# Performance work log

Measured on AMD Instinct MI355X. Metric: run time of the kernel, lower is better.

The kernel has to match this reference:

```python
import jax, jax.numpy as jnp
import numpy as np

B, LQ, LK, D = 32, 2048, 2048, 64


def setup_inputs() -> dict:
    key = jax.random.key(0)
    k1, k2, k3, k4 = jax.random.split(key, 4)
    querys = jax.random.normal(k1, (B, LQ, D), dtype=jnp.float32)
    keys = jax.random.normal(k2, (B, LK, D), dtype=jnp.float32)
    values = jax.random.normal(k3, (B, LK, D), dtype=jnp.float32)
    # valid lengths in [1, LK]
    valid_lens = jax.random.randint(k4, (B,), 1, LK + 1, dtype=jnp.int32)
    return {"querys": querys, "keys": keys, "values": values, "valid_lens": valid_lens}


def reference(querys, keys, values, valid_lens):
    d = querys.shape[-1]
    # [B, Lq, Lk] score matrix
    scores = jnp.einsum("bqd,bkd->bqk", querys, keys) / jnp.sqrt(jnp.asarray(d, querys.dtype))
    # masked softmax: key positions >= valid_len get -1e6 (as in d2l masked_softmax)
    key_pos = jnp.arange(scores.shape[-1], dtype=jnp.int32)  # [Lk]
    mask = key_pos[None, None, :] < valid_lens[:, None, None]  # [B, 1, Lk]
    scores = jnp.where(mask, scores, jnp.asarray(-1e6, scores.dtype))
    attn = jax.nn.softmax(scores, axis=-1)
    # dropout p=0.0 -> identity
    return jnp.einsum("bqk,bkd->bqd", attn, values)
```

## Files before the change

### kernel.cpp

```cpp
#include <hip/hip_runtime.h>
#include <hip/hip_bf16.h>
#include <math.h>


#define B_    32
#define LQ_   2048
#define LK_   2048
#define D_    64

typedef __attribute__((ext_vector_type(8)))  short bf16x8;
typedef __attribute__((ext_vector_type(4)))  float f32x4;
typedef __attribute__((ext_vector_type(16))) float f32x16;
typedef __attribute__((ext_vector_type(2)))  unsigned u32x2;

static __device__ __forceinline__ unsigned pk_bf16(float a, float b) {
    __hip_bfloat162 h = __float22bfloat162_rn(float2{a, b});
    return *(unsigned*)&h;
}

static __device__ __forceinline__ u32x2 plswap(unsigned a, unsigned b) {
    return __builtin_amdgcn_permlane32_swap(a, b, false, false);
}
static __device__ __forceinline__ float xhalf_max(float x) {
    u32x2 r = plswap(__float_as_uint(x), __float_as_uint(x));
    return fmaxf(__uint_as_float(r[0]), __uint_as_float(r[1]));
}
static __device__ __forceinline__ float xhalf_add(float x) {
    u32x2 r = plswap(__float_as_uint(x), __float_as_uint(x));
    return __uint_as_float(r[0]) + __uint_as_float(r[1]);
}

template<int NS>
__global__ __launch_bounds__(256, 2) void fa_split9_kernel(
    const float* __restrict__ Q, const float* __restrict__ K,
    const float* __restrict__ V, const int* __restrict__ vlen,
    float* __restrict__ OP, float* __restrict__ ML)
{
    __shared__ __align__(16) short Kl[2][64 * 64];
    __shared__ __align__(16) short Vt[2][64 * 64];

    const int tid  = threadIdx.x;
    const int wid  = tid >> 6;
    const int lane = tid & 63;
    const int c31  = lane & 31;
    const int h    = lane >> 5;

    constexpr int PB = 16 * NS;
    const int L    = blockIdx.x;
    const int rank = L / PB;
    const int sub  = L % PB;
    const int qb   = sub & 15;
    const int s    = sub >> 4;
    int b;
    {
        const int vj = vlen[c31];
        int r = 0;
#pragma unroll
        for (int k = 0; k < 32; ++k) {
            const int vk = __shfl(vj, k);
            r += (vk > vj) || (vk == vj && k < c31);
        }
        const unsigned long long match = __ballot(r == rank);
        b = (int)(__ffsll((unsigned long long)match) - 1) & 31;
    }
    const int q0 = qb * 128 + wid * 32;
    const int vl = vlen[b];
    const int nt    = (vl + 63) >> 6;
    const int chunk = (nt + NS - 1) / NS;
    const int t0    = s * chunk;
    const int t1    = min(t0 + chunk, nt);

    const float qscale = 0.125f * 1.44269504088896340736f;

    unsigned qfrag[4][4];
#pragma unroll
    for (int ks = 0; ks < 4; ++ks) {
        const float* qp = Q + ((size_t)(b * LQ_ + q0 + c31)) * D_ + ks * 16 + h * 8;
        f32x4 t0v = *(const f32x4*)qp;
        f32x4 t1v = *(const f32x4*)(qp + 4);
#pragma unroll
        for (int jj = 0; jj < 2; ++jj) {
            qfrag[ks][jj]     = pk_bf16(t0v[2*jj] * qscale, t0v[2*jj+1] * qscale);
            qfrag[ks][jj + 2] = pk_bf16(t1v[2*jj] * qscale, t1v[2*jj+1] * qscale);
        }
    }

    f32x16 oacc[2];
#pragma unroll
    for (int dt = 0; dt < 2; ++dt)
#pragma unroll
        for (int r = 0; r < 16; ++r) oacc[dt][r] = 0.f;
    float mrun = -INFINITY, lrun = 0.f;

    const int skey = tid >> 2, skh = tid & 3;
    const int vkg = tid >> 4, vdg = tid & 15;

    const float* kgp = K + ((size_t)(b * LK_ + skey)) * D_ + skh * 16;
    const float* vgp = V + ((size_t)(b * LK_ + vkg * 4)) * D_ + vdg * 4;

    f32x4 kr[4], vr[4];
    if (t0 < t1) {
        const size_t off = (size_t)t0 * 64 * D_;
#pragma unroll
        for (int i = 0; i < 4; ++i) kr[i] = *(const f32x4*)(kgp + off + 4 * i);
#pragma unroll
        for (int i = 0; i < 4; ++i) vr[i] = *(const f32x4*)(vgp + off + (size_t)i * D_);
    }

    for (int t = t0; t < t1; ++t) {
        const int k0 = t * 64;
        const int buf = t & 1;

        {
            unsigned pk32[8];
#pragma unroll
            for (int m = 0; m < 8; ++m)
                pk32[m] = pk_bf16(kr[m >> 1][2 * (m & 1)], kr[m >> 1][2 * (m & 1) + 1]);
#pragma unroll
            for (int cch = 0; cch < 2; ++cch) {
                const int pos = (skh * 2 + cch) ^ (skey & 7);
                *(bf16x8*)&Kl[buf][skey * 64 + pos * 8] = *(bf16x8*)&pk32[4 * cch];
            }
#pragma unroll
            for (int dr = 0; dr < 4; ++dr) {
                const unsigned w0 = pk_bf16(vr[0][dr], vr[1][dr]);
                const unsigned w1 = pk_bf16(vr[2][dr], vr[3][dr]);
                const int dim = vdg * 4 + dr;
                const int pos = (vkg >> 1) ^ (dim & 7);
                uint2* dst = (uint2*)&Vt[buf][dim * 64 + pos * 8 + (vkg & 1) * 4];
                *dst = uint2{w0, w1};
            }
        }
        __syncthreads();

        if (t + 1 < t1) {
            const float* kn = kgp + (size_t)(k0 + 64) * D_;
            const float* vn = vgp + (size_t)(k0 + 64) * D_;
#pragma unroll
            for (int i = 0; i < 4; ++i) kr[i] = *(const f32x4*)(kn + 4 * i);
#pragma unroll
            for (int i = 0; i < 4; ++i) vr[i] = *(const f32x4*)(vn + (size_t)i * D_);
        }

        f32x16 st[2];
#pragma unroll
        for (int ss = 0; ss < 2; ++ss) {
#pragma unroll
            for (int r = 0; r < 16; ++r) st[ss][r] = 0.f;
#pragma unroll
            for (int ks = 0; ks < 4; ++ks) {
                const int pos = (ks * 2 + h) ^ (c31 & 7);
                bf16x8 kf = *(const bf16x8*)&Kl[buf][(ss * 32 + c31) * 64 + pos * 8];
                st[ss] = __builtin_amdgcn_mfma_f32_32x32x16_bf16(
                    kf, *(const bf16x8*)&qfrag[ks][0], st[ss], 0, 0, 0);
            }
        }

        if (k0 + 64 > vl) {
#pragma unroll
            for (int ss = 0; ss < 2; ++ss) {
                const int base = k0 + ss * 32 + 4 * h;
#pragma unroll
                for (int r = 0; r < 16; ++r) {
                    const int key = base + (r & 3) + 8 * (r >> 2);
                    if (key >= vl) st[ss][r] = -1e30f;
                }
            }
        }

        float m8[8];
#pragma unroll
        for (int r = 0; r < 8; ++r)
            m8[r] = fmaxf(fmaxf(st[0][r], st[0][r + 8]),
                          fmaxf(st[1][r], st[1][r + 8]));
#pragma unroll
        for (int o = 4; o; o >>= 1)
#pragma unroll
            for (int r = 0; r < o; ++r) m8[r] = fmaxf(m8[r], m8[r + o]);
        const float tm = xhalf_max(m8[0]);

        if (__any(tm > mrun + 8.f)) {
            const float mnew = fmaxf(mrun, tm);
            const float corr = exp2f(mrun - mnew);
            lrun *= corr;
#pragma unroll
            for (int dt = 0; dt < 2; ++dt)
#pragma unroll
                for (int r = 0; r < 16; ++r) oacc[dt][r] *= corr;
            mrun = mnew;
        }
#pragma unroll
        for (int ss = 0; ss < 2; ++ss)
#pragma unroll
            for (int r = 0; r < 16; ++r)
                st[ss][r] = exp2f(st[ss][r] - mrun);
        float s8[8];
#pragma unroll
        for (int r = 0; r < 8; ++r)
            s8[r] = (st[0][r] + st[0][r + 8]) + (st[1][r] + st[1][r + 8]);
#pragma unroll
        for (int o = 4; o; o >>= 1)
#pragma unroll
            for (int r = 0; r < o; ++r) s8[r] += s8[r + o];
        lrun += xhalf_add(s8[0]);

        unsigned pk[2][8];
#pragma unroll
        for (int ss = 0; ss < 2; ++ss)
#pragma unroll
            for (int m = 0; m < 8; ++m)
                pk[ss][m] = pk_bf16(st[ss][2 * m], st[ss][2 * m + 1]);

#pragma unroll
        for (int kq = 0; kq < 4; ++kq) {
            const int ss = kq >> 1, A4 = (kq & 1) * 4;
            u32x2 r02 = plswap(pk[ss][A4],     pk[ss][A4 + 2]);
            u32x2 r13 = plswap(pk[ss][A4 + 1], pk[ss][A4 + 3]);
            unsigned pf[4] = {r02[0], r13[0], r02[1], r13[1]};
            const bf16x8 pfr = *(const bf16x8*)&pf[0];
#pragma unroll
            for (int dt = 0; dt < 2; ++dt) {
                const int pos = (kq * 2 + h) ^ (c31 & 7);
                bf16x8 vf = *(const bf16x8*)&Vt[buf][(dt * 32 + c31) * 64 + pos * 8];
                oacc[dt] = __builtin_amdgcn_mfma_f32_32x32x16_bf16(vf, pfr, oacc[dt], 0, 0, 0);
            }
        }
    }

    const size_t row = (size_t)s * (B_ * LQ_) + b * LQ_ + q0 + c31;
    float* op = OP + row * D_;
#pragma unroll
    for (int dt = 0; dt < 2; ++dt)
#pragma unroll
        for (int g = 0; g < 4; ++g) {
            f32x4 v;
#pragma unroll
            for (int j = 0; j < 4; ++j) v[j] = oacc[dt][4 * g + j];
            *(f32x4*)(op + dt * 32 + 8 * g + 4 * h) = v;
        }
    if (h == 0)
        *(float2*)&ML[row * 2] = float2{mrun, lrun};
}

template<int NS>
__global__ __launch_bounds__(256) void fa_merge_kernel(
    const float* __restrict__ OP, const float* __restrict__ ML,
    float* __restrict__ O)
{
    const int g   = blockIdx.x * 256 + threadIdx.x;
    const int row = g >> 4;
    const int qd  = (g & 15) * 4;

    float mf = -INFINITY;
#pragma unroll
    for (int s = 0; s < NS; ++s) {
        float2 ml = *(const float2*)&ML[((size_t)s * (B_ * LQ_) + row) * 2];
        mf = fmaxf(mf, ml.x);
    }
    float den = 0.f;
    f32x4 acc = {0.f, 0.f, 0.f, 0.f};
#pragma unroll
    for (int s = 0; s < NS; ++s) {
        const size_t srow = (size_t)s * (B_ * LQ_) + row;
        float2 ml = *(const float2*)&ML[srow * 2];
        const float c = exp2f(ml.x - mf);
        den += c * ml.y;
        f32x4 v = *(const f32x4*)&OP[srow * D_ + qd];
        acc += v * c;
    }
    const float inv = 1.f / den;
    *(f32x4*)(O + (size_t)row * D_ + qd) = acc * inv;
}

__global__ __launch_bounds__(128, 2) void fa_mono_kernel(
    const float* __restrict__ Q, const float* __restrict__ K,
    const float* __restrict__ V, const int* __restrict__ vlen,
    float* __restrict__ O)
{
    __shared__ __align__(16) short Kl[2][64 * 64];
    __shared__ __align__(16) short Vt[2][64 * 64];

    const int tid  = threadIdx.x;
    const int wave = tid >> 6;
    const int lane = tid & 63;
    const int c31  = lane & 31;
    const int h    = lane >> 5;

    const int b  = blockIdx.y;
    const int q0 = blockIdx.x * 64 + wave * 32;
    const int vl = vlen[b];
    const int nt = (vl + 63) >> 6;

    const float qscale = 0.125f * 1.44269504088896340736f;

    unsigned qfrag[4][4];
#pragma unroll
    for (int ks = 0; ks < 4; ++ks) {
        const float* qp = Q + ((size_t)(b * LQ_ + q0 + c31)) * D_ + ks * 16 + h * 8;
        f32x4 t0 = *(const f32x4*)qp;
        f32x4 t1 = *(const f32x4*)(qp + 4);
#pragma unroll
        for (int jj = 0; jj < 2; ++jj) {
            qfrag[ks][jj]     = pk_bf16(t0[2*jj] * qscale, t0[2*jj+1] * qscale);
            qfrag[ks][jj + 2] = pk_bf16(t1[2*jj] * qscale, t1[2*jj+1] * qscale);
        }
    }

    f32x16 oacc[2];
#pragma unroll
    for (int dt = 0; dt < 2; ++dt)
#pragma unroll
        for (int r = 0; r < 16; ++r) oacc[dt][r] = 0.f;
    float mrun = -INFINITY, lrun = 0.f;

    const int skey = tid >> 1, skh = tid & 1;
    const int vkg = tid >> 4, vdg = tid & 15;

    const float* kgp = K + ((size_t)(b * LK_ + skey)) * D_ + skh * 32;
    const float* vgp = V + ((size_t)(b * LK_ + vkg * 8)) * D_ + vdg * 4;

    f32x4 kr[8], vr[8];
#pragma unroll
    for (int i = 0; i < 8; ++i) kr[i] = *(const f32x4*)(kgp + 4 * i);
#pragma unroll
    for (int i = 0; i < 8; ++i) vr[i] = *(const f32x4*)(vgp + (size_t)i * D_);

    for (int t = 0; t < nt; ++t) {
        const int k0 = t * 64;
        const int buf = t & 1;
        {
            unsigned pk32[16];
#pragma unroll
            for (int m = 0; m < 16; ++m)
                pk32[m] = pk_bf16(kr[m >> 1][2 * (m & 1)], kr[m >> 1][2 * (m & 1) + 1]);
#pragma unroll
            for (int cch = 0; cch < 4; ++cch) {
                const int pos = (skh * 4 + cch) ^ (skey & 7);
                *(bf16x8*)&Kl[buf][skey * 64 + pos * 8] = *(bf16x8*)&pk32[4 * cch];
            }
#pragma unroll
            for (int dr = 0; dr < 4; ++dr) {
                unsigned w[4];
#pragma unroll
                for (int p = 0; p < 4; ++p)
                    w[p] = pk_bf16(vr[2 * p][dr], vr[2 * p + 1][dr]);
                const int dim = vdg * 4 + dr;
                const int pos = vkg ^ (dim & 7);
                *(bf16x8*)&Vt[buf][dim * 64 + pos * 8] = *(bf16x8*)&w[0];
            }
        }
        if (t + 1 < nt) {
            const float* kn = kgp + (size_t)(k0 + 64) * D_;
            const float* vn = vgp + (size_t)(k0 + 64) * D_;
#pragma unroll
            for (int i = 0; i < 8; ++i) kr[i] = *(const f32x4*)(kn + 4 * i);
#pragma unroll
            for (int i = 0; i < 8; ++i) vr[i] = *(const f32x4*)(vn + (size_t)i * D_);
        }
        __syncthreads();

        f32x16 st[2];
#pragma unroll
        for (int ss = 0; ss < 2; ++ss) {
#pragma unroll
            for (int r = 0; r < 16; ++r) st[ss][r] = 0.f;
#pragma unroll
            for (int ks = 0; ks < 4; ++ks) {
                const int pos = (ks * 2 + h) ^ (c31 & 7);
                bf16x8 kf = *(const bf16x8*)&Kl[buf][(ss * 32 + c31) * 64 + pos * 8];
                st[ss] = __builtin_amdgcn_mfma_f32_32x32x16_bf16(
                    kf, *(const bf16x8*)&qfrag[ks][0], st[ss], 0, 0, 0);
            }
        }
        if (k0 + 64 > vl) {
#pragma unroll
            for (int ss = 0; ss < 2; ++ss) {
                const int base = k0 + ss * 32 + 4 * h;
#pragma unroll
                for (int r = 0; r < 16; ++r) {
                    const int key = base + (r & 3) + 8 * (r >> 2);
                    if (key >= vl) st[ss][r] = -1e30f;
                }
            }
        }
        float tm = st[0][0];
#pragma unroll
        for (int ss = 0; ss < 2; ++ss)
#pragma unroll
            for (int r = 0; r < 16; ++r) tm = fmaxf(tm, st[ss][r]);
        tm = fmaxf(tm, __shfl_xor(tm, 32));
        if (__any(tm > mrun + 8.f)) {
            const float mnew = fmaxf(mrun, tm);
            const float corr = exp2f(mrun - mnew);
            lrun *= corr;
#pragma unroll
            for (int dt = 0; dt < 2; ++dt)
#pragma unroll
                for (int r = 0; r < 16; ++r) oacc[dt][r] *= corr;
            mrun = mnew;
        }
        float rs = 0.f;
#pragma unroll
        for (int ss = 0; ss < 2; ++ss)
#pragma unroll
            for (int r = 0; r < 16; ++r) {
                const float p = exp2f(st[ss][r] - mrun);
                st[ss][r] = p;
                rs += p;
            }
        rs += __shfl_xor(rs, 32);
        lrun += rs;

        unsigned pk[2][8];
#pragma unroll
        for (int ss = 0; ss < 2; ++ss)
#pragma unroll
            for (int m = 0; m < 8; ++m)
                pk[ss][m] = pk_bf16(st[ss][2 * m], st[ss][2 * m + 1]);
#pragma unroll
        for (int kq = 0; kq < 4; ++kq) {
            const int ss = kq >> 1, A4 = (kq & 1) * 4;
            unsigned p0 = pk[ss][A4], p1 = pk[ss][A4+1], p2 = pk[ss][A4+2], p3 = pk[ss][A4+3];
            unsigned xp0 = __shfl_xor((int)p0, 32);
            unsigned xp1 = __shfl_xor((int)p1, 32);
            unsigned xp2 = __shfl_xor((int)p2, 32);
            unsigned xp3 = __shfl_xor((int)p3, 32);
            unsigned pf[4];
            pf[0] = h ? xp2 : p0;
            pf[1] = h ? xp3 : p1;
            pf[2] = h ? p2  : xp0;
            pf[3] = h ? p3  : xp1;
            const bf16x8 pfr = *(const bf16x8*)&pf[0];
#pragma unroll
            for (int dt = 0; dt < 2; ++dt) {
                const int pos = (kq * 2 + h) ^ (c31 & 7);
                bf16x8 vf = *(const bf16x8*)&Vt[buf][(dt * 32 + c31) * 64 + pos * 8];
                oacc[dt] = __builtin_amdgcn_mfma_f32_32x32x16_bf16(vf, pfr, oacc[dt], 0, 0, 0);
            }
        }
    }

    const float inv = 1.f / lrun;
    float* op = O + ((size_t)(b * LQ_ + q0 + c31)) * D_;
#pragma unroll
    for (int dt = 0; dt < 2; ++dt)
#pragma unroll
        for (int g = 0; g < 4; ++g) {
            f32x4 v;
#pragma unroll
            for (int j = 0; j < 4; ++j) v[j] = oacc[dt][4 * g + j] * inv;
            *(f32x4*)(op + dt * 32 + 8 * g + 4 * h) = v;
        }
}

extern "C" void kernel_launch(void* const* d_in, const int* in_sizes, int n_in,
                              void* d_out, int out_size, void* d_ws, size_t ws_size,
                              hipStream_t stream) {
    const float* Q    = (const float*)d_in[0];
    const float* K    = (const float*)d_in[1];
    const float* V    = (const float*)d_in[2];
    const int*   vlen = (const int*)d_in[3];
    float*       O    = (float*)d_out;

    const size_t rows = (size_t)B_ * LQ_;
    auto need = [&](int ns) { return (size_t)ns * rows * (D_ + 2) * sizeof(float); };

    int NS = 0;
    if      (d_ws && ws_size >= need(4)) NS = 4;
    else if (d_ws && ws_size >= need(2)) NS = 2;
    else if (d_ws && ws_size >= need(1)) NS = 1;

    if (NS == 0) {
        dim3 grid(LQ_ / 64, B_);
        fa_mono_kernel<<<grid, dim3(128), 0, stream>>>(Q, K, V, vlen, O);
        return;
    }

    float* OP = (float*)d_ws;
    float* ML = (float*)d_ws + (size_t)NS * rows * D_;

    const unsigned nblk = (unsigned)(16 * B_ * NS);
    switch (NS) {
        case 4: fa_split9_kernel<4><<<dim3(nblk), dim3(256), 0, stream>>>(Q, K, V, vlen, OP, ML); break;
        case 2: fa_split9_kernel<2><<<dim3(nblk), dim3(256), 0, stream>>>(Q, K, V, vlen, OP, ML); break;
        default: fa_split9_kernel<1><<<dim3(nblk), dim3(256), 0, stream>>>(Q, K, V, vlen, OP, ML); break;
    }

    dim3 g2((unsigned)((rows * (D_ / 4)) / 256));
    switch (NS) {
        case 4: fa_merge_kernel<4><<<g2, dim3(256), 0, stream>>>(OP, ML, O); break;
        case 2: fa_merge_kernel<2><<<g2, dim3(256), 0, stream>>>(OP, ML, O); break;
        default: fa_merge_kernel<1><<<g2, dim3(256), 0, stream>>>(OP, ML, O); break;
    }
}
```

Baseline: 153.0 us.

## Pre-convert K/V to bf16 and transposed V, load MFMA fragments directly from global

Adds a preprocessing kernel that converts K to bf16 and V to a transposed bf16 layout in workspace. A new attention kernel then has each wave load its MFMA operand fragments straight from global or L2, with no LDS staging and no __syncthreads. Each wave now owns a single 32-row query tile, with occupancy hinted at 4 blocks. This removes repeated per-block fp32-to-bf16 conversion and LDS traffic, but each wave re-reads K/V from cache, adds an extra launch, and needs a larger workspace to hold the bf16 copies.

```diff
diff --git a/kernel.cpp b/kernel.cpp
--- a/kernel.cpp
+++ b/kernel.cpp
@@ -28,6 +28,247 @@
 static __device__ __forceinline__ float xhalf_add(float x) {
     u32x2 r = plswap(__float_as_uint(x), __float_as_uint(x));
     return __uint_as_float(r[0]) + __uint_as_float(r[1]);
+}
+
+__global__ __launch_bounds__(256) void fa_cvt_kernel(
+    const float* __restrict__ K, const float* __restrict__ V,
+    short* __restrict__ Kb, short* __restrict__ Vtb)
+{
+    const int tid = threadIdx.x;
+    const int b   = blockIdx.y;
+    const int k0  = blockIdx.x * 64;
+
+    {
+        const int kk = tid >> 2, q4 = tid & 3;
+        const size_t off = ((size_t)(b * LK_ + k0 + kk)) * D_ + q4 * 16;
+        const float* src = K + off;
+        unsigned w[8];
+#pragma unroll
+        for (int i = 0; i < 4; ++i) {
+            f32x4 v = *(const f32x4*)(src + 4 * i);
+            w[2 * i]     = pk_bf16(v[0], v[1]);
+            w[2 * i + 1] = pk_bf16(v[2], v[3]);
+        }
+        short* dst = Kb + off;
+        *(bf16x8*)dst       = *(bf16x8*)&w[0];
+        *(bf16x8*)(dst + 8) = *(bf16x8*)&w[4];
+    }
+    {
+        const int vkg = tid & 15, vdg = tid >> 4;
+        f32x4 vv[4];
+#pragma unroll
+        for (int p = 0; p < 4; ++p)
+            vv[p] = *(const f32x4*)&V[((size_t)(b * LK_ + k0 + vkg * 4 + p)) * D_ + vdg * 4];
+#pragma unroll
+        for (int dr = 0; dr < 4; ++dr) {
+            uint2 w = { pk_bf16(vv[0][dr], vv[1][dr]), pk_bf16(vv[2][dr], vv[3][dr]) };
+            *(uint2*)&Vtb[((size_t)(b * 64 + vdg * 4 + dr)) * LK_ + k0 + vkg * 4] = w;
+        }
+    }
+}
+
+template<int NS>
+__global__ __launch_bounds__(256, 4) void fa_frag_kernel(
+    const float* __restrict__ Q, const short* __restrict__ Kb,
+    const short* __restrict__ Vtb, const int* __restrict__ vlen,
+    float* __restrict__ OP, float* __restrict__ ML)
+{
+    const int tid  = threadIdx.x;
+    const int wid  = tid >> 6;
+    const int lane = tid & 63;
+    const int c31  = lane & 31;
+    const int h    = lane >> 5;
+
+    constexpr int PB = 64 * NS;
+    const int T    = blockIdx.x * 4 + wid;
+    const int rank = T / PB;
+    const int sub  = T % PB;
+    const int qw   = sub & 63;
+    const int s    = sub >> 6;
+    int b;
+    {
+        const int vj = vlen[c31];
+        int r = 0;
+#pragma unroll
+        for (int k = 0; k < 32; ++k) {
+            const int vk = __shfl(vj, k);
+            r += (vk > vj) || (vk == vj && k < c31);
+        }
+        const unsigned long long match = __ballot(r == rank);
+        b = (int)(__ffsll(match) - 1) & 31;
+    }
+    const int q0 = qw * 32;
+    const int vl = vlen[b];
+    const int nt    = (vl + 63) >> 6;
+    const int chunk = (nt + NS - 1) / NS;
+    const int t0    = s * chunk;
+    const int t1    = min(t0 + chunk, nt);
+
+    const float qscale = 0.125f * 1.44269504088896340736f;
+
+    unsigned qfrag[4][4];
+#pragma unroll
+    for (int ks = 0; ks < 4; ++ks) {
+        const float* qp = Q + ((size_t)(b * LQ_ + q0 + c31)) * D_ + ks * 16 + h * 8;
+        f32x4 t0v = *(const f32x4*)qp;
+        f32x4 t1v = *(const f32x4*)(qp + 4);
+#pragma unroll
+        for (int jj = 0; jj < 2; ++jj) {
+            qfrag[ks][jj]     = pk_bf16(t0v[2*jj] * qscale, t0v[2*jj+1] * qscale);
+            qfrag[ks][jj + 2] = pk_bf16(t1v[2*jj] * qscale, t1v[2*jj+1] * qscale);
+        }
+    }
+
+    f32x16 oacc[2];
+#pragma unroll
+    for (int dt = 0; dt < 2; ++dt)
+#pragma unroll
+        for (int r = 0; r < 16; ++r) oacc[dt][r] = 0.f;
+    float mrun = -INFINITY, lrun = 0.f;
+
+    const short* kb  = Kb  + (size_t)b * LK_ * D_;
+    const short* vtb = Vtb + (size_t)b * D_ * LK_;
+
+    for (int t = t0; t < t1; ++t) {
+        const int k0 = t * 64;
+
+        bf16x8 kf[2][4];
+#pragma unroll
+        for (int ss = 0; ss < 2; ++ss)
+#pragma unroll
+            for (int ks = 0; ks < 4; ++ks)
+                kf[ss][ks] = *(const bf16x8*)&kb[((size_t)(k0 + ss * 32 + c31)) * D_ + ks * 16 + h * 8];
+
+        f32x16 st[2];
+#pragma unroll
+        for (int ss = 0; ss < 2; ++ss) {
+#pragma unroll
+            for (int r = 0; r < 16; ++r) st[ss][r] = 0.f;
+#pragma unroll
+            for (int ks = 0; ks < 4; ++ks)
+                st[ss] = __builtin_amdgcn_mfma_f32_32x32x16_bf16(
+                    kf[ss][ks], *(const bf16x8*)&qfrag[ks][0], st[ss], 0, 0, 0);
+        }
+
+        bf16x8 vf[2][4];
+#pragma unroll
+        for (int dt = 0; dt < 2; ++dt)
+#pragma unroll
+            for (int kq = 0; kq < 4; ++kq)
+                vf[dt][kq] = *(const bf16x8*)&vtb[((size_t)(dt * 32 + c31)) * LK_ + k0 + kq * 16 + h * 8];
+
+        if (k0 + 64 > vl) {
+#pragma unroll
+            for (int ss = 0; ss < 2; ++ss) {
+                const int base = k0 + ss * 32 + 4 * h;
+#pragma unroll
+                for (int r = 0; r < 16; ++r) {
+                    const int key = base + (r & 3) + 8 * (r >> 2);
+                    if (key >= vl) st[ss][r] = -1e30f;
+                }
+            }
+        }
+
+        float m8[8];
+#pragma unroll
+        for (int r = 0; r < 8; ++r)
+            m8[r] = fmaxf(fmaxf(st[0][r], st[0][r + 8]),
+                          fmaxf(st[1][r], st[1][r + 8]));
+#pragma unroll
+        for (int o = 4; o; o >>= 1)
+#pragma unroll
+            for (int r = 0; r < o; ++r) m8[r] = fmaxf(m8[r], m8[r + o]);
+        const float tm = xhalf_max(m8[0]);
+
+        if (__any(tm > mrun + 8.f)) {
+            const float mnew = fmaxf(mrun, tm);
+            const float corr = exp2f(mrun - mnew);
+            lrun *= corr;
+#pragma unroll
+            for (int dt = 0; dt < 2; ++dt)
+#pragma unroll
+                for (int r = 0; r < 16; ++r) oacc[dt][r] *= corr;
+            mrun = mnew;
+        }
+#pragma unroll
+        for (int ss = 0; ss < 2; ++ss)
+#pragma unroll
+            for (int r = 0; r < 16; ++r)
+                st[ss][r] = exp2f(st[ss][r] - mrun);
+        float s8[8];
+#pragma unroll
+        for (int r = 0; r < 8; ++r)
+            s8[r] = (st[0][r] + st[0][r + 8]) + (st[1][r] + st[1][r + 8]);
+#pragma unroll
+        for (int o = 4; o; o >>= 1)
+#pragma unroll
+            for (int r = 0; r < o; ++r) s8[r] += s8[r + o];
+        lrun += xhalf_add(s8[0]);
+
+        unsigned pk[2][8];
+#pragma unroll
+        for (int ss = 0; ss < 2; ++ss)
+#pragma unroll
+            for (int m = 0; m < 8; ++m)
+                pk[ss][m] = pk_bf16(st[ss][2 * m], st[ss][2 * m + 1]);
+
+#pragma unroll
+        for (int kq = 0; kq < 4; ++kq) {
+            const int ss = kq >> 1, A4 = (kq & 1) * 4;
+            u32x2 r02 = plswap(pk[ss][A4],     pk[ss][A4 + 2]);
+            u32x2 r13 = plswap(pk[ss][A4 + 1], pk[ss][A4 + 3]);
+            unsigned pf[4] = {r02[0], r13[0], r02[1], r13[1]};
+            const bf16x8 pfr = *(const bf16x8*)&pf[0];
+#pragma unroll
+            for (int dt = 0; dt < 2; ++dt)
+                oacc[dt] = __builtin_amdgcn_mfma_f32_32x32x16_bf16(
+                    vf[dt][kq], pfr, oacc[dt], 0, 0, 0);
+        }
+    }
+
+    const size_t row = (size_t)s * (B_ * LQ_) + b * LQ_ + q0 + c31;
+    float* op = OP + row * D_;
+#pragma unroll
+    for (int dt = 0; dt < 2; ++dt)
+#pragma unroll
+        for (int g = 0; g < 4; ++g) {
+            f32x4 v;
+#pragma unroll
+            for (int j = 0; j < 4; ++j) v[j] = oacc[dt][4 * g + j];
+            *(f32x4*)(op + dt * 32 + 8 * g + 4 * h) = v;
+        }
+    if (h == 0)
+        *(float2*)&ML[row * 2] = float2{mrun, lrun};
+}
+
+template<int NS>
+__global__ __launch_bounds__(256) void fa_merge_kernel(
+    const float* __restrict__ OP, const float* __restrict__ ML,
+    float* __restrict__ O)
+{
+    const int g   = blockIdx.x * 256 + threadIdx.x;
+    const int row = g >> 4;
+    const int qd  = (g & 15) * 4;
+
+    float mf = -INFINITY;
+#pragma unroll
+    for (int s = 0; s < NS; ++s) {
+        float2 ml = *(const float2*)&ML[((size_t)s * (B_ * LQ_) + row) * 2];
+        mf = fmaxf(mf, ml.x);
+    }
+    float den = 0.f;
+    f32x4 acc = {0.f, 0.f, 0.f, 0.f};
+#pragma unroll
+    for (int s = 0; s < NS; ++s) {
+        const size_t srow = (size_t)s * (B_ * LQ_) + row;
+        float2 ml = *(const float2*)&ML[srow * 2];
+        const float c = exp2f(ml.x - mf);
+        den += c * ml.y;
+        f32x4 v = *(const f32x4*)&OP[srow * D_ + qd];
+        acc += v * c;
+    }
+    const float inv = 1.f / den;
+    *(f32x4*)(O + (size_t)row * D_ + qd) = acc * inv;
 }
 
 template<int NS>
@@ -61,7 +302,7 @@
             r += (vk > vj) || (vk == vj && k < c31);
         }
         const unsigned long long match = __ballot(r == rank);
-        b = (int)(__ffsll((unsigned long long)match) - 1) & 31;
+        b = (int)(__ffsll(match) - 1) & 31;
     }
     const int q0 = qb * 128 + wid * 32;
     const int vl = vlen[b];
@@ -110,7 +351,6 @@
     for (int t = t0; t < t1; ++t) {
         const int k0 = t * 64;
         const int buf = t & 1;
-
         {
             unsigned pk32[8];
 #pragma unroll
@@ -127,12 +367,10 @@
                 const unsigned w1 = pk_bf16(vr[2][dr], vr[3][dr]);
                 const int dim = vdg * 4 + dr;
                 const int pos = (vkg >> 1) ^ (dim & 7);
-                uint2* dst = (uint2*)&Vt[buf][dim * 64 + pos * 8 + (vkg & 1) * 4];
-                *dst = uint2{w0, w1};
+                *(uint2*)&Vt[buf][dim * 64 + pos * 8 + (vkg & 1) * 4] = uint2{w0, w1};
             }
         }
         __syncthreads();
-
         if (t + 1 < t1) {
             const float* kn = kgp + (size_t)(k0 + 64) * D_;
             const float* vn = vgp + (size_t)(k0 + 64) * D_;
@@ -155,7 +393,6 @@
                     kf, *(const bf16x8*)&qfrag[ks][0], st[ss], 0, 0, 0);
             }
         }
-
         if (k0 + 64 > vl) {
 #pragma unroll
             for (int ss = 0; ss < 2; ++ss) {
@@ -167,7 +404,6 @@
                 }
             }
         }
-
         float m8[8];
 #pragma unroll
         for (int r = 0; r < 8; ++r)
@@ -178,7 +414,6 @@
 #pragma unroll
             for (int r = 0; r < o; ++r) m8[r] = fmaxf(m8[r], m8[r + o]);
         const float tm = xhalf_max(m8[0]);
-
         if (__any(tm > mrun + 8.f)) {
             const float mnew = fmaxf(mrun, tm);
             const float corr = exp2f(mrun - mnew);
@@ -210,7 +445,6 @@
 #pragma unroll
             for (int m = 0; m < 8; ++m)
                 pk[ss][m] = pk_bf16(st[ss][2 * m], st[ss][2 * m + 1]);
-
 #pragma unroll
         for (int kq = 0; kq < 4; ++kq) {
             const int ss = kq >> 1, A4 = (kq & 1) * 4;
@@ -221,8 +455,8 @@
 #pragma unroll
             for (int dt = 0; dt < 2; ++dt) {
                 const int pos = (kq * 2 + h) ^ (c31 & 7);
-                bf16x8 vf = *(const bf16x8*)&Vt[buf][(dt * 32 + c31) * 64 + pos * 8];
-                oacc[dt] = __builtin_amdgcn_mfma_f32_32x32x16_bf16(vf, pfr, oacc[dt], 0, 0, 0);
+                bf16x8 vfv = *(const bf16x8*)&Vt[buf][(dt * 32 + c31) * 64 + pos * 8];
+                oacc[dt] = __builtin_amdgcn_mfma_f32_32x32x16_bf16(vfv, pfr, oacc[dt], 0, 0, 0);
             }
         }
     }
@@ -240,36 +474,6 @@
         }
     if (h == 0)
         *(float2*)&ML[row * 2] = float2{mrun, lrun};
-}
-
-template<int NS>
-__global__ __launch_bounds__(256) void fa_merge_kernel(
-    const float* __restrict__ OP, const float* __restrict__ ML,
-    float* __restrict__ O)
-{
-    const int g   = blockIdx.x * 256 + threadIdx.x;
-    const int row = g >> 4;
-    const int qd  = (g & 15) * 4;
-
-    float mf = -INFINITY;
-#pragma unroll
-    for (int s = 0; s < NS; ++s) {
-        float2 ml = *(const float2*)&ML[((size_t)s * (B_ * LQ_) + row) * 2];
-        mf = fmaxf(mf, ml.x);
-    }
-    float den = 0.f;
-    f32x4 acc = {0.f, 0.f, 0.f, 0.f};
-#pragma unroll
-    for (int s = 0; s < NS; ++s) {
-        const size_t srow = (size_t)s * (B_ * LQ_) + row;
-        float2 ml = *(const float2*)&ML[srow * 2];
-        const float c = exp2f(ml.x - mf);
-        den += c * ml.y;
-        f32x4 v = *(const f32x4*)&OP[srow * D_ + qd];
-        acc += v * c;
-    }
-    const float inv = 1.f / den;
-    *(f32x4*)(O + (size_t)row * D_ + qd) = acc * inv;
 }
 
 __global__ __launch_bounds__(128, 2) void fa_mono_kernel(
@@ -462,34 +666,39 @@
     const int*   vlen = (const int*)d_in[3];
     float*       O    = (float*)d_out;
 
-    const size_t rows = (size_t)B_ * LQ_;
-    auto need = [&](int ns) { return (size_t)ns * rows * (D_ + 2) * sizeof(float); };
-
-    int NS = 0;
-    if      (d_ws && ws_size >= need(4)) NS = 4;
-    else if (d_ws && ws_size >= need(2)) NS = 2;
-    else if (d_ws && ws_size >= need(1)) NS = 1;
-
-    if (NS == 0) {
-        dim3 grid(LQ_ / 64, B_);
-        fa_mono_kernel<<<grid, dim3(128), 0, stream>>>(Q, K, V, vlen, O);
+    const size_t rows    = (size_t)B_ * LQ_;
+    const size_t kvElems = (size_t)B_ * LK_ * D_;
+    auto needP = [&](int ns) { return (size_t)ns * rows * (D_ + 2) * sizeof(float); };
+    const size_t needKV = 2 * kvElems * sizeof(short);
+
+    constexpr int NS = 4;
+
+    if (d_ws && ws_size >= needP(NS) + needKV) {
+        float* OP  = (float*)d_ws;
+        float* ML  = OP + (size_t)NS * rows * D_;
+        short* Kb  = (short*)(ML + (size_t)NS * rows * 2);
+        short* Vtb = Kb + kvElems;
+
+        fa_cvt_kernel<<<dim3(LK_ / 64, B_), dim3(256), 0, stream>>>(K, V, Kb, Vtb);
+
+        const unsigned nblk = (unsigned)(64 * B_ * NS / 4);
+        fa_frag_kernel<NS><<<dim3(nblk), dim3(256), 0, stream>>>(Q, Kb, Vtb, vlen, OP, ML);
+
+        dim3 g2((unsigned)((rows * (D_ / 4)) / 256));
+        fa_merge_kernel<NS><<<g2, dim3(256), 0, stream>>>(OP, ML, O);
         return;
     }
 
-    float* OP = (float*)d_ws;
-    float* ML = (float*)d_ws + (size_t)NS * rows * D_;
-
-    const unsigned nblk = (unsigned)(16 * B_ * NS);
-    switch (NS) {
-        case 4: fa_split9_kernel<4><<<dim3(nblk), dim3(256), 0, stream>>>(Q, K, V, vlen, OP, ML); break;
-        case 2: fa_split9_kernel<2><<<dim3(nblk), dim3(256), 0, stream>>>(Q, K, V, vlen, OP, ML); break;
-        default: fa_split9_kernel<1><<<dim3(nblk), dim3(256), 0, stream>>>(Q, K, V, vlen, OP, ML); break;
-    }
-
-    dim3 g2((unsigned)((rows * (D_ / 4)) / 256));
-    switch (NS) {
-        case 4: fa_merge_kernel<4><<<g2, dim3(256), 0, stream>>>(OP, ML, O); break;
-        case 2: fa_merge_kernel<2><<<g2, dim3(256), 0, stream>>>(OP, ML, O); break;
-        default: fa_merge_kernel<1><<<g2, dim3(256), 0, stream>>>(OP, ML, O); break;
-    }
-}
+    if (d_ws && ws_size >= needP(NS)) {
+        float* OP = (float*)d_ws;
+        float* ML = OP + (size_t)NS * rows * D_;
+        const unsigned nblk = (unsigned)(16 * B_ * NS);
+        fa_split9_kernel<NS><<<dim3(nblk), dim3(256), 0, stream>>>(Q, K, V, vlen, OP, ML);
+        dim3 g2((unsigned)((rows * (D_ / 4)) / 256));
+        fa_merge_kernel<NS><<<g2, dim3(256), 0, stream>>>(OP, ML, O);
+        return;
+    }
+
+    dim3 grid(LQ_ / 64, B_);
+    fa_mono_kernel<<<grid, dim3(128), 0, stream>>>(Q, K, V, vlen, O);
+}
```

After: 210.0 us. 1.37x slower.
